# Performance work log

Hardware: AMD Instinct MI355X
Metric: run time of the kernel (lower is better)

The kernel has to match this reference:

```python
import jax, jax.numpy as jnp
import numpy as np

B, S, HID = 1, 2048, 4096
NH, NKV, HD = 32, 8, 128
GROUPS = NH // NKV
ROPE_THETA = 10000.0


def rotate_half(x):
    x1, x2 = jnp.split(x, 2, axis=-1)
    return jnp.concatenate([-x2, x1], axis=-1)


def rope_cos_sin(position_ids, head_dim, dtype):
    # inv_freq: [hd/2]; position_ids: [B, S]
    inv_freq = 1.0 / (ROPE_THETA ** (jnp.arange(0, head_dim, 2, dtype=jnp.float32) / head_dim))
    freqs = position_ids.astype(jnp.float32)[..., None] * inv_freq  # [B, S, hd/2]
    emb = jnp.concatenate([freqs, freqs], axis=-1)                  # [B, S, hd]
    return jnp.cos(emb).astype(dtype), jnp.sin(emb).astype(dtype)


def apply_rope(x, cos, sin):
    # x: [B, H, S, hd]; cos/sin: [B, S, hd] -> broadcast over heads
    return x * cos[:, None] + rotate_half(x) * sin[:, None]


def setup_inputs() -> dict:
    key = jax.random.key(0)
    ks = jax.random.split(key, 5)
    scale = 0.02
    return {
        "hidden_states": jax.random.normal(ks[0], (B, S, HID), dtype=jnp.float32),
        "wq": jax.random.normal(ks[1], (HID, NH * HD), dtype=jnp.float32) * scale,
        "wk": jax.random.normal(ks[2], (HID, NKV * HD), dtype=jnp.float32) * scale,
        "wv": jax.random.normal(ks[3], (HID, NKV * HD), dtype=jnp.float32) * scale,
        "wo": jax.random.normal(ks[4], (NH * HD, HID), dtype=jnp.float32) * scale,
        "position_ids": jnp.arange(S, dtype=jnp.int32)[None, :],
    }


def reference(hidden_states, wq, wk, wv, wo, position_ids):
    bsz, q_len, _ = hidden_states.shape
    # projections (nn.Linear, bias=False)
    q = (hidden_states @ wq).reshape(bsz, q_len, NH, HD).transpose(0, 2, 1, 3)   # [B,NH,S,hd]
    k = (hidden_states @ wk).reshape(bsz, q_len, NKV, HD).transpose(0, 2, 1, 3)  # [B,NKV,S,hd]
    v = (hidden_states @ wv).reshape(bsz, q_len, NKV, HD).transpose(0, 2, 1, 3)
    # RoPE applied to Q and K at global positions (prefill: no past cache)
    cos, sin = rope_cos_sin(position_ids, HD, q.dtype)
    q = apply_rope(q, cos, sin)
    k = apply_rope(k, cos, sin)
    # GQA: expand KV heads to query heads
    k_full = jnp.repeat(k, GROUPS, axis=1)  # [B,NH,S,hd]
    v_full = jnp.repeat(v, GROUPS, axis=1)
    # prefill flash attention == causal SDPA
    logits = jnp.einsum('bhqd,bhkd->bhqk', q, k_full) / jnp.sqrt(jnp.asarray(HD, q.dtype))
    causal = jnp.tril(jnp.ones((q_len, q_len), dtype=bool))
    neg = jnp.asarray(jnp.finfo(q.dtype).min, q.dtype)
    logits = jnp.where(causal[None, None], logits, neg)
    probs = jax.nn.softmax(logits, axis=-1)                     # [B,NH,S,S]
    attn = jnp.einsum('bhqk,bhkd->bhqd', probs, v_full)          # [B,NH,S,hd]
    attn_output = attn.transpose(0, 2, 1, 3).reshape(bsz, q_len, NH * HD) @ wo
    # chunked prefill eviction scores: causal attention probs accumulated over
    # all queries, aggregated per KV head group -> [B, NKV, kv_len]
    accumulated_scores = probs.sum(axis=2).reshape(bsz, NKV, GROUPS, q_len).sum(axis=2)
    return attn_output, accumulated_scores
```

## Files before the change

kernel.cpp:

```cpp
#include <hip/hip_runtime.h>
#include <hip/hip_bf16.h>
#include <cstdint>
#include <cstddef>

#define S_LEN 2048
#define HID_DIM 4096
#define NH 32
#define NKV 8
#define HD 128
#define LOG2E 1.4426950408889634f
#define SCALE 0.08838834764831845f

typedef __attribute__((ext_vector_type(8))) short bf16x8;
typedef __attribute__((ext_vector_type(4))) float f32x4;
typedef __attribute__((ext_vector_type(16))) float f32x16;
typedef __attribute__((ext_vector_type(4))) short short4v;
typedef __attribute__((ext_vector_type(4))) unsigned u32x4;

__device__ __forceinline__ short f2bf(float f) {
  union { float f; unsigned u; } v; v.f = f;
  return (short)((v.u + 0x7fffu + ((v.u >> 16) & 1u)) >> 16);
}
__device__ __forceinline__ float bf2f(short s) {
  union { unsigned u; float f; } v; v.u = ((unsigned)(unsigned short)s) << 16;
  return v.f;
}
__device__ __forceinline__ unsigned cvt_pk_bf16(float lo, float hi) {
  unsigned r;
  asm("v_cvt_pk_bf16_f32 %0, %1, %2" : "=v"(r) : "v"(lo), "v"(hi));
  return r;
}
__device__ __forceinline__ void gld_lds16(const void* g, void* l) {
  __builtin_amdgcn_global_load_lds((const __attribute__((address_space(1))) unsigned*)g,
                                   (__attribute__((address_space(3))) unsigned*)l, 16, 0, 0);
}

#define WAITVM8() asm volatile("s_waitcnt vmcnt(8)" ::: "memory")
#define WAITVM4() asm volatile("s_waitcnt vmcnt(4)" ::: "memory")
#define WAITVM0() asm volatile("s_waitcnt vmcnt(0)" ::: "memory")

__global__ void cvt_kernel(const float* __restrict__ in, short* __restrict__ out, int n) {
  int i = (blockIdx.x * 256 + threadIdx.x) * 4;
  if (i < n) {
    float4 f = *(const float4*)(in + i);
    short4v o = { f2bf(f.x), f2bf(f.y), f2bf(f.z), f2bf(f.w) };
    *(short4v*)(out + i) = o;
  }
}

__global__ void tconv_kernel(const float* __restrict__ in, short* __restrict__ out, int R, int C) {
  __shared__ float tile[32][33];
  int tr = blockIdx.y * 32, tc = blockIdx.x * 32;
  int tx = threadIdx.x & 31, ty = threadIdx.x >> 5;
#pragma unroll
  for (int i = 0; i < 32; i += 8)
    tile[ty + i][tx] = in[(size_t)(tr + ty + i) * C + tc + tx];
  __syncthreads();
#pragma unroll
  for (int i = 0; i < 32; i += 8)
    out[(size_t)(tc + ty + i) * R + tr + tx] = f2bf(tile[tx][ty + i]);
}

template<int MODE>
__global__ __launch_bounds__(256, 4) void gemm_bt_kernel(
    const short* __restrict__ A, const short* __restrict__ Bt,
    void* __restrict__ Cout, int M, int N, int K, int rchunk, int cchunk)
{
  __shared__ short As[2][128 * 32];
  __shared__ short Bs[2][128 * 32];
  const int tid = threadIdx.x;
  const int lane = tid & 63;
  const int w = tid >> 6;
  const int wm = w >> 1, wn = w & 1;
  const int xcd = blockIdx.x & 7;
  const int local = blockIdx.x >> 3;
  const int by = (xcd >> 2) * rchunk + (local % rchunk);
  const int bx = (xcd & 3) * cchunk + (local / rchunk);
  const int m0 = by * 128, n0 = bx * 128;

  auto stage = [&](int bb, int k0) {
#pragma unroll
    for (int rep = 0; rep < 2; rep++) {
      int c = rep * 256 + tid;
      int row = c >> 2, slot = c & 3;
      int gs = slot ^ (row & 3);
      gld_lds16(A + (size_t)(m0 + row) * K + k0 + gs * 8, &As[bb][c * 8]);
      gld_lds16(Bt + (size_t)(n0 + row) * K + k0 + gs * 8, &Bs[bb][c * 8]);
    }
  };

  f32x4 acc[4][4];
#pragma unroll
  for (int i = 0; i < 4; i++)
#pragma unroll
    for (int j = 0; j < 4; j++) acc[i][j] = (f32x4){0.f, 0.f, 0.f, 0.f};

  const int NT = K >> 5;
  stage(0, 0);
  for (int kt = 0; kt < NT; kt++) {
    const int b = kt & 1;
    if (kt + 1 < NT) { stage(b ^ 1, (kt + 1) << 5); WAITVM4(); }
    else             { WAITVM0(); }
    __builtin_amdgcn_s_barrier();

    bf16x8 af[4], bf[4];
#pragma unroll
    for (int ms = 0; ms < 4; ms++) {
      int row = wm * 64 + ms * 16 + (lane & 15);
      af[ms] = *(const bf16x8*)(&As[b][row * 32 + (((lane >> 4) ^ (row & 3)) << 3)]);
    }
#pragma unroll
    for (int ns = 0; ns < 4; ns++) {
      int row = wn * 64 + ns * 16 + (lane & 15);
      bf[ns] = *(const bf16x8*)(&Bs[b][row * 32 + (((lane >> 4) ^ (row & 3)) << 3)]);
    }
#pragma unroll
    for (int ms = 0; ms < 4; ms++)
#pragma unroll
      for (int ns = 0; ns < 4; ns++)
        acc[ms][ns] = __builtin_amdgcn_mfma_f32_16x16x32_bf16(af[ms], bf[ns], acc[ms][ns], 0, 0, 0);

    __builtin_amdgcn_s_barrier();
  }

#pragma unroll
  for (int ms = 0; ms < 4; ms++) {
    int mb = m0 + wm * 64 + ms * 16 + ((lane >> 4) << 2);
#pragma unroll
    for (int ns = 0; ns < 4; ns++) {
      int n = n0 + wn * 64 + ns * 16 + (lane & 15);
      if (MODE == 3) {
        short* o = (short*)Cout;
        if (n < NH * HD) {
          int head = n >> 7, d = n & 127;
#pragma unroll
          for (int r = 0; r < 4; r++)
            o[((size_t)head * M + (mb + r)) * HD + d] = f2bf(acc[ms][ns][r]);
        } else if (n < (NH + NKV) * HD) {
          int head = (n - NH * HD) >> 7, d = n & 127;
          short* ok = o + (size_t)NH * S_LEN * HD;
#pragma unroll
          for (int r = 0; r < 4; r++)
            ok[((size_t)head * M + (mb + r)) * HD + d] = f2bf(acc[ms][ns][r]);
        } else {
          int head = (n - (NH + NKV) * HD) >> 7, d = n & 127;
          short* ov = o + (size_t)(NH + NKV) * S_LEN * HD;
          short4v pk;
#pragma unroll
          for (int r = 0; r < 4; r++) pk[r] = f2bf(acc[ms][ns][r]);
          *(short4v*)(ov + ((size_t)head * HD + d) * M + mb) = pk;
        }
      } else {
        float* o = (float*)Cout;
#pragma unroll
        for (int r = 0; r < 4; r++)
          o[(size_t)(mb + r) * N + n] = acc[ms][ns][r];
      }
    }
  }
}

__global__ void rope_kernel(short* __restrict__ q, short* __restrict__ k,
                            const int* __restrict__ pos_ids) {
  const int s = blockIdx.x;
  const int hh = blockIdx.y * 4 + threadIdx.y;
  const int d = threadIdx.x;
  const float pos = (float)pos_ids[s];
  const float inv = __expf(-(float)d * 0.14391157f);
  float sn, c;
  __sincosf(pos * inv, &sn, &c);
  short* base = (hh < NH) ? (q + ((size_t)hh * S_LEN + s) * HD)
                          : (k + ((size_t)(hh - NH) * S_LEN + s) * HD);
  float x1 = bf2f(base[d]), x2 = bf2f(base[d + 64]);
  base[d] = f2bf(x1 * c - x2 * sn);
  base[d + 64] = f2bf(x2 * c + x1 * sn);
}

__global__ __launch_bounds__(256, 2) void attn_kernel(
    const short* __restrict__ Qr, const short* __restrict__ Kr, const short* __restrict__ Vt,
    short* __restrict__ attn_out, float* __restrict__ scores)
{
  __shared__ short Ks[2][64 * 128];
  __shared__ short Vs[2][128 * 64];
  __shared__ float cs[2048];

  const int tid = threadIdx.x;
  const int lane = tid & 63;
  const int w = tid >> 6;
  const int h2 = lane >> 5;
  const int l31 = lane & 31;
  const int xcd = blockIdx.x & 7;
  const int j = blockIdx.x >> 3;
  const int qt = (j < 32) ? (15 - (j >> 2)) : ((j - 32) >> 2);
  const int h = xcd * 4 + (j & 3);
  const int kvh = xcd;
  const float CS = SCALE * LOG2E;

  const short* KrB = Kr + (size_t)kvh * S_LEN * HD;
  const short* VtB = Vt + (size_t)kvh * HD * S_LEN;

  for (int i = tid; i < 2048; i += 256) cs[i] = 0.f;

  auto stageK = [&](int bb, int t) {
    const int kb2 = t * 64;
#pragma unroll
    for (int rep = 0; rep < 4; rep++) {
      int c = rep * 256 + tid;
      int x = c >> 4, slot = c & 15;
      int key = (x & 0x33) | ((x & 4) << 1) | ((x & 8) >> 1);
      int gs = slot ^ (x & 7);
      gld_lds16(KrB + (size_t)(kb2 + key) * HD + gs * 8, &Ks[bb][c * 8]);
    }
  };
  auto stageV = [&](int bb, int t) {
    const int kb2 = t * 64;
#pragma unroll
    for (int rep = 0; rep < 4; rep++) {
      int c = rep * 256 + tid;
      int d = c >> 3, slot = c & 7;
      int gs = slot ^ (d & 7);
      gld_lds16(VtB + (size_t)d * S_LEN + kb2 + gs * 8, &Vs[bb][c * 8]);
    }
  };

  const int nt = 2 * qt + 2;
  const int qbase = qt * 128 + w * 32;
  const int qglob = qbase + l31;
  const int qmaxw = qbase + 31;

  bf16x8 qf[8];
  {
    const short* qrow = Qr + ((size_t)h * S_LEN + qglob) * HD + h2 * 8;
#pragma unroll
    for (int kc = 0; kc < 8; kc++) qf[kc] = *(const bf16x8*)(qrow + kc * 16);
  }

  f32x16 oacc[4];
#pragma unroll
  for (int i = 0; i < 4; i++) oacc[i] = (f32x16)(0.f);
  float lsum = 0.f;

  stageK(0, 0); stageV(0, 0);
  for (int t = 0; t < nt; t++) {
    const int b = t & 1;
    const int kb = t * 64;
    if (t + 1 < nt) { stageK(b ^ 1, t + 1); stageV(b ^ 1, t + 1); WAITVM8(); }
    else            { WAITVM0(); }
    __builtin_amdgcn_s_barrier();

    if (kb <= qmaxw) {
      f32x16 sf[2];
      sf[0] = (f32x16)(0.f); sf[1] = (f32x16)(0.f);
      __builtin_amdgcn_s_setprio(1);
#pragma unroll
      for (int kc = 0; kc < 8; kc++)
#pragma unroll
        for (int bl = 0; bl < 2; bl++) {
          int x = bl * 32 + l31;
          bf16x8 kf = *(const bf16x8*)(&Ks[b][x * 128 + (((kc * 2 + h2) ^ (lane & 7)) << 3)]);
          sf[bl] = __builtin_amdgcn_mfma_f32_32x32x16_bf16(kf, qf[kc], sf[bl], 0, 0, 0);
        }
      __builtin_amdgcn_s_setprio(0);

      float p[2][16];
      const bool diag = (kb + 63 > qbase);
#pragma unroll
      for (int bl = 0; bl < 2; bl++)
#pragma unroll
        for (int a = 0; a < 4; a++)
#pragma unroll
          for (int cc = 0; cc < 4; cc++) {
            float pv = exp2f(sf[bl][a * 4 + cc] * CS);
            if (diag) {
              int key = kb + bl * 32 + (a >> 1) * 16 + h2 * 8 + (a & 1) * 4 + cc;
              if (key > qglob) pv = 0.f;
            }
            p[bl][a * 4 + cc] = pv;
            lsum += pv;
          }

      bf16x8 pa[4];
#pragma unroll
      for (int s = 0; s < 4; s++) {
        const int bl = s >> 1, base = 8 * (s & 1);
        u32x4 pw;
        pw[0] = cvt_pk_bf16(p[bl][base + 0], p[bl][base + 1]);
        pw[1] = cvt_pk_bf16(p[bl][base + 2], p[bl][base + 3]);
        pw[2] = cvt_pk_bf16(p[bl][base + 4], p[bl][base + 5]);
        pw[3] = cvt_pk_bf16(p[bl][base + 6], p[bl][base + 7]);
        pa[s] = __builtin_bit_cast(bf16x8, pw);
      }

      __builtin_amdgcn_s_setprio(1);
#pragma unroll
      for (int s = 0; s < 4; s++)
#pragma unroll
        for (int db = 0; db < 4; db++) {
          int d = db * 32 + l31;
          bf16x8 vf = *(const bf16x8*)(&Vs[b][d * 64 + (((s * 2 + h2) ^ (lane & 7)) << 3)]);
          oacc[db] = __builtin_amdgcn_mfma_f32_32x32x16_bf16(pa[s], vf, oacc[db], 0, 0, 0);
        }
      __builtin_amdgcn_s_setprio(0);
    }
    __builtin_amdgcn_s_barrier();
  }

  lsum += __shfl_xor(lsum, 32);
  float rlv = 1.f / lsum;
  float rl16[16];
#pragma unroll
  for (int r = 0; r < 16; r++)
    rl16[r] = __shfl(rlv, (r & 3) + 8 * (r >> 2) + 4 * h2);

#pragma unroll
  for (int db = 0; db < 4; db++) {
    int d = db * 32 + l31;
#pragma unroll
    for (int r = 0; r < 16; r++) {
      int qq = qbase + (r & 3) + 8 * (r >> 2) + 4 * h2;
      attn_out[(size_t)qq * HID_DIM + h * HD + d] = f2bf(oacc[db][r] * rl16[r]);
    }
  }

  const int xl = (l31 & 0x13) | ((l31 & 4) << 1) | ((l31 & 8) >> 1);
  stageK(0, 0);
  for (int t = 0; t < nt; t++) {
    const int b = t & 1;
    const int kb = t * 64;
    if (t + 1 < nt) { stageK(b ^ 1, t + 1); WAITVM4(); }
    else            { WAITVM0(); }
    __builtin_amdgcn_s_barrier();

    if (kb <= qmaxw) {
      f32x16 sg[2];
      sg[0] = (f32x16)(0.f); sg[1] = (f32x16)(0.f);
      __builtin_amdgcn_s_setprio(1);
#pragma unroll
      for (int kc = 0; kc < 8; kc++)
#pragma unroll
        for (int bl = 0; bl < 2; bl++) {
          int x = bl * 32 + xl;
          bf16x8 kf = *(const bf16x8*)(&Ks[b][x * 128 + (((kc * 2 + h2) ^ (x & 7)) << 3)]);
          sg[bl] = __builtin_amdgcn_mfma_f32_32x32x16_bf16(qf[kc], kf, sg[bl], 0, 0, 0);
        }
      __builtin_amdgcn_s_setprio(0);

      const bool diag = (kb + 63 > qbase);
#pragma unroll
      for (int bl = 0; bl < 2; bl++) {
        int key = kb + bl * 32 + l31;
        float sum = 0.f;
#pragma unroll
        for (int r = 0; r < 16; r++) {
          float pv = exp2f(sg[bl][r] * CS) * rl16[r];
          if (diag && key > qbase + (r & 3) + 8 * (r >> 2) + 4 * h2) pv = 0.f;
          sum += pv;
        }
        sum += __shfl_xor(sum, 32);
        if (lane < 32) atomicAdd(&cs[key], sum);
      }
    }
    __builtin_amdgcn_s_barrier();
  }

  asm volatile("s_waitcnt lgkmcnt(0)" ::: "memory");
  __builtin_amdgcn_s_barrier();
  const int nk = nt * 64;
  for (int i = tid; i < nk; i += 256)
    atomicAdd(scores + (size_t)kvh * S_LEN + i, cs[i]);
}

extern "C" void kernel_launch(void* const* d_in, const int* in_sizes, int n_in,
                              void* d_out, int out_size, void* d_ws, size_t ws_size,
                              hipStream_t stream) {
  const float* hs = (const float*)d_in[0];
  const float* wq = (const float*)d_in[1];
  const float* wk = (const float*)d_in[2];
  const float* wv = (const float*)d_in[3];
  const float* wo = (const float*)d_in[4];
  const int* pos = (const int*)d_in[5];
  float* out = (float*)d_out;

  char* ws = (char*)d_ws;
  const size_t off_hs   = 0;
  const size_t off_wqT  = off_hs   + (size_t)S_LEN * HID_DIM * 2;
  const size_t off_wkT  = off_wqT  + (size_t)HID_DIM * HID_DIM * 2;
  const size_t off_wvT  = off_wkT  + (size_t)1024 * HID_DIM * 2;
  const size_t off_woT  = off_wvT  + (size_t)1024 * HID_DIM * 2;
  const size_t off_Qr   = off_woT  + (size_t)HID_DIM * HID_DIM * 2;
  const size_t off_Kr   = off_Qr   + (size_t)NH * S_LEN * HD * 2;
  const size_t off_Vt   = off_Kr   + (size_t)NKV * S_LEN * HD * 2;
  const size_t off_attn = off_Vt   + (size_t)NKV * HD * S_LEN * 2;

  short* hsb  = (short*)(ws + off_hs);
  short* wqT  = (short*)(ws + off_wqT);
  short* wkT  = (short*)(ws + off_wkT);
  short* wvT  = (short*)(ws + off_wvT);
  short* woT  = (short*)(ws + off_woT);
  short* Qr   = (short*)(ws + off_Qr);
  short* Kr   = (short*)(ws + off_Kr);
  short* Vt   = (short*)(ws + off_Vt);
  short* attb = (short*)(ws + off_attn);

  cvt_kernel<<<dim3((S_LEN * HID_DIM) / 1024), 256, 0, stream>>>(hs, hsb, S_LEN * HID_DIM);
  tconv_kernel<<<dim3(128, 128), 256, 0, stream>>>(wq, wqT, HID_DIM, HID_DIM);
  tconv_kernel<<<dim3(32, 128), 256, 0, stream>>>(wk, wkT, HID_DIM, 1024);
  tconv_kernel<<<dim3(32, 128), 256, 0, stream>>>(wv, wvT, HID_DIM, 1024);
  tconv_kernel<<<dim3(128, 128), 256, 0, stream>>>(wo, woT, HID_DIM, HID_DIM);

  gemm_bt_kernel<3><<<768, 256, 0, stream>>>(hsb, wqT, Qr, S_LEN, 6144, HID_DIM, 8, 12);

  rope_kernel<<<dim3(S_LEN, 10), dim3(64, 4), 0, stream>>>(Qr, Kr, pos);

  hipMemsetAsync(out + (size_t)S_LEN * HID_DIM, 0, (size_t)NKV * S_LEN * sizeof(float), stream);
  attn_kernel<<<512, 256, 0, stream>>>(Qr, Kr, Vt, attb, out + (size_t)S_LEN * HID_DIM);

  gemm_bt_kernel<2><<<512, 256, 0, stream>>>(attb, woT, out, S_LEN, HID_DIM, HID_DIM, 8, 8);
}
```

Before: 401.7 us.

## Split attention block into paired 64-row q-tiles with key-split waves

Each block now handles two 64-row query tiles (one long and one short, paired so causal work is balanced) instead of one 128-row tile. Each tile's waves are split two ways over query rows and two ways over the keys of every 64-key tile. The partial O and row sums are combined through LDS, which reuses the K/V buffers. The score pass now reads K straight from global memory, with waves striding over key tiles, instead of staging it in LDS. This trades extra LDS reduction, barriers and uncached-pattern global K reads for finer-grained causal balance and smaller per-wave MFMA chains.

```diff
diff --git a/kernel.cpp b/kernel.cpp
--- a/kernel.cpp
+++ b/kernel.cpp
@@ -187,12 +187,14 @@
   const int tid = threadIdx.x;
   const int lane = tid & 63;
   const int w = tid >> 6;
+  const int r = w & 1;
+  const int kh = w >> 1;
   const int h2 = lane >> 5;
   const int l31 = lane & 31;
   const int xcd = blockIdx.x & 7;
   const int j = blockIdx.x >> 3;
-  const int qt = (j < 32) ? (15 - (j >> 2)) : ((j - 32) >> 2);
   const int h = xcd * 4 + (j & 3);
+  const int p = j >> 2;
   const int kvh = xcd;
   const float CS = SCALE * LOG2E;
 
@@ -200,6 +202,10 @@
   const short* VtB = Vt + (size_t)kvh * HD * S_LEN;
 
   for (int i = tid; i < 2048; i += 256) cs[i] = 0.f;
+
+  float* obuf = (float*)Ks;
+  float* lbuf = (float*)Vs;
+  float* rlbuf = lbuf + 64;
 
   auto stageK = [&](int bb, int t) {
     const int kb2 = t * 64;
@@ -223,115 +229,130 @@
     }
   };
 
-  const int nt = 2 * qt + 2;
-  const int qbase = qt * 128 + w * 32;
-  const int qglob = qbase + l31;
-  const int qmaxw = qbase + 31;
-
-  bf16x8 qf[8];
-  {
-    const short* qrow = Qr + ((size_t)h * S_LEN + qglob) * HD + h2 * 8;
-#pragma unroll
-    for (int kc = 0; kc < 8; kc++) qf[kc] = *(const bf16x8*)(qrow + kc * 16);
-  }
-
-  f32x16 oacc[4];
-#pragma unroll
-  for (int i = 0; i < 4; i++) oacc[i] = (f32x16)(0.f);
-  float lsum = 0.f;
-
-  stageK(0, 0); stageV(0, 0);
-  for (int t = 0; t < nt; t++) {
-    const int b = t & 1;
-    const int kb = t * 64;
-    if (t + 1 < nt) { stageK(b ^ 1, t + 1); stageV(b ^ 1, t + 1); WAITVM8(); }
-    else            { WAITVM0(); }
-    __builtin_amdgcn_s_barrier();
-
-    if (kb <= qmaxw) {
-      f32x16 sf[2];
-      sf[0] = (f32x16)(0.f); sf[1] = (f32x16)(0.f);
-      __builtin_amdgcn_s_setprio(1);
-#pragma unroll
-      for (int kc = 0; kc < 8; kc++)
-#pragma unroll
-        for (int bl = 0; bl < 2; bl++) {
-          int x = bl * 32 + l31;
-          bf16x8 kf = *(const bf16x8*)(&Ks[b][x * 128 + (((kc * 2 + h2) ^ (lane & 7)) << 3)]);
-          sf[bl] = __builtin_amdgcn_mfma_f32_32x32x16_bf16(kf, qf[kc], sf[bl], 0, 0, 0);
-        }
-      __builtin_amdgcn_s_setprio(0);
-
-      float p[2][16];
-      const bool diag = (kb + 63 > qbase);
-#pragma unroll
-      for (int bl = 0; bl < 2; bl++)
+  for (int sidx = 0; sidx < 2; sidx++) {
+    const int qt = sidx ? p : (31 - p);
+    const int nt = qt + 1;
+    const int qbase = qt * 64 + r * 32;
+    const int qglob = qbase + l31;
+    const int qmaxw = qbase + 31;
+
+    bf16x8 qf[8];
+    {
+      const short* qrow = Qr + ((size_t)h * S_LEN + qglob) * HD + h2 * 8;
+#pragma unroll
+      for (int kc = 0; kc < 8; kc++) qf[kc] = *(const bf16x8*)(qrow + kc * 16);
+    }
+
+    f32x16 oacc[4];
+#pragma unroll
+    for (int i = 0; i < 4; i++) oacc[i] = (f32x16)(0.f);
+    float lsum = 0.f;
+
+    stageK(0, 0); stageV(0, 0);
+    for (int t = 0; t < nt; t++) {
+      const int b = t & 1;
+      const int kb = t * 64;
+      if (t + 1 < nt) { stageK(b ^ 1, t + 1); stageV(b ^ 1, t + 1); WAITVM8(); }
+      else            { WAITVM0(); }
+      __builtin_amdgcn_s_barrier();
+
+      if (kb <= qmaxw) {
+        f32x16 sf = (f32x16)(0.f);
+        const int x = kh * 32 + l31;
+        __builtin_amdgcn_s_setprio(1);
+#pragma unroll
+        for (int kc = 0; kc < 8; kc++) {
+          bf16x8 kf = *(const bf16x8*)(&Ks[b][x * 128 + (((kc * 2 + h2) ^ (x & 7)) << 3)]);
+          sf = __builtin_amdgcn_mfma_f32_32x32x16_bf16(kf, qf[kc], sf, 0, 0, 0);
+        }
+        __builtin_amdgcn_s_setprio(0);
+
+        float pv16[16];
+        const bool diag = (kb + 63 > qbase);
 #pragma unroll
         for (int a = 0; a < 4; a++)
 #pragma unroll
           for (int cc = 0; cc < 4; cc++) {
-            float pv = exp2f(sf[bl][a * 4 + cc] * CS);
+            float pv = exp2f(sf[a * 4 + cc] * CS);
             if (diag) {
-              int key = kb + bl * 32 + (a >> 1) * 16 + h2 * 8 + (a & 1) * 4 + cc;
+              int key = kb + kh * 32 + (a >> 1) * 16 + h2 * 8 + (a & 1) * 4 + cc;
               if (key > qglob) pv = 0.f;
             }
-            p[bl][a * 4 + cc] = pv;
+            pv16[a * 4 + cc] = pv;
             lsum += pv;
           }
 
-      bf16x8 pa[4];
-#pragma unroll
-      for (int s = 0; s < 4; s++) {
-        const int bl = s >> 1, base = 8 * (s & 1);
-        u32x4 pw;
-        pw[0] = cvt_pk_bf16(p[bl][base + 0], p[bl][base + 1]);
-        pw[1] = cvt_pk_bf16(p[bl][base + 2], p[bl][base + 3]);
-        pw[2] = cvt_pk_bf16(p[bl][base + 4], p[bl][base + 5]);
-        pw[3] = cvt_pk_bf16(p[bl][base + 6], p[bl][base + 7]);
-        pa[s] = __builtin_bit_cast(bf16x8, pw);
+        bf16x8 pa[2];
+#pragma unroll
+        for (int s = 0; s < 2; s++) {
+          u32x4 pw;
+          pw[0] = cvt_pk_bf16(pv16[8 * s + 0], pv16[8 * s + 1]);
+          pw[1] = cvt_pk_bf16(pv16[8 * s + 2], pv16[8 * s + 3]);
+          pw[2] = cvt_pk_bf16(pv16[8 * s + 4], pv16[8 * s + 5]);
+          pw[3] = cvt_pk_bf16(pv16[8 * s + 6], pv16[8 * s + 7]);
+          pa[s] = __builtin_bit_cast(bf16x8, pw);
+        }
+
+        __builtin_amdgcn_s_setprio(1);
+#pragma unroll
+        for (int s = 0; s < 2; s++) {
+          const int g = kh * 2 + s;
+#pragma unroll
+          for (int db = 0; db < 4; db++) {
+            int d = db * 32 + l31;
+            bf16x8 vf = *(const bf16x8*)(&Vs[b][d * 64 + (((g * 2 + h2) ^ (d & 7)) << 3)]);
+            oacc[db] = __builtin_amdgcn_mfma_f32_32x32x16_bf16(pa[s], vf, oacc[db], 0, 0, 0);
+          }
+        }
+        __builtin_amdgcn_s_setprio(0);
       }
-
-      __builtin_amdgcn_s_setprio(1);
-#pragma unroll
-      for (int s = 0; s < 4; s++)
-#pragma unroll
-        for (int db = 0; db < 4; db++) {
-          int d = db * 32 + l31;
-          bf16x8 vf = *(const bf16x8*)(&Vs[b][d * 64 + (((s * 2 + h2) ^ (lane & 7)) << 3)]);
-          oacc[db] = __builtin_amdgcn_mfma_f32_32x32x16_bf16(pa[s], vf, oacc[db], 0, 0, 0);
-        }
-      __builtin_amdgcn_s_setprio(0);
+      __builtin_amdgcn_s_barrier();
+    }
+
+    lsum += __shfl_xor(lsum, 32);
+    if (kh == 0) {
+#pragma unroll
+      for (int db = 0; db < 4; db++)
+#pragma unroll
+        for (int r16 = 0; r16 < 16; r16++) {
+          int crow = (r16 & 3) + 8 * (r16 >> 2) + 4 * h2;
+          obuf[(r * 32 + crow) * 128 + db * 32 + l31] = oacc[db][r16];
+        }
+      if (lane < 32) lbuf[r * 32 + l31] = lsum;
     }
     __builtin_amdgcn_s_barrier();
-  }
-
-  lsum += __shfl_xor(lsum, 32);
-  float rlv = 1.f / lsum;
-  float rl16[16];
-#pragma unroll
-  for (int r = 0; r < 16; r++)
-    rl16[r] = __shfl(rlv, (r & 3) + 8 * (r >> 2) + 4 * h2);
-
-#pragma unroll
-  for (int db = 0; db < 4; db++) {
-    int d = db * 32 + l31;
-#pragma unroll
-    for (int r = 0; r < 16; r++) {
-      int qq = qbase + (r & 3) + 8 * (r >> 2) + 4 * h2;
-      attn_out[(size_t)qq * HID_DIM + h * HD + d] = f2bf(oacc[db][r] * rl16[r]);
-    }
-  }
-
-  const int xl = (l31 & 0x13) | ((l31 & 4) << 1) | ((l31 & 8) >> 1);
-  stageK(0, 0);
-  for (int t = 0; t < nt; t++) {
-    const int b = t & 1;
-    const int kb = t * 64;
-    if (t + 1 < nt) { stageK(b ^ 1, t + 1); WAITVM4(); }
-    else            { WAITVM0(); }
+
+    if (kh == 1) {
+      float ltot = lsum + lbuf[r * 32 + l31];
+      float rlv = 1.f / ltot;
+      float rl16[16];
+#pragma unroll
+      for (int r16 = 0; r16 < 16; r16++)
+        rl16[r16] = __shfl(rlv, (r16 & 3) + 8 * (r16 >> 2) + 4 * h2);
+#pragma unroll
+      for (int db = 0; db < 4; db++) {
+        int d = db * 32 + l31;
+#pragma unroll
+        for (int r16 = 0; r16 < 16; r16++) {
+          int crow = (r16 & 3) + 8 * (r16 >> 2) + 4 * h2;
+          float o = oacc[db][r16] + obuf[(r * 32 + crow) * 128 + d];
+          attn_out[(size_t)(qbase + crow) * HID_DIM + h * HD + d] = f2bf(o * rl16[r16]);
+        }
+      }
+      if (lane < 32) rlbuf[r * 32 + l31] = rlv;
+    }
     __builtin_amdgcn_s_barrier();
 
-    if (kb <= qmaxw) {
+    float rlv = rlbuf[r * 32 + l31];
+    float rl16[16];
+#pragma unroll
+    for (int r16 = 0; r16 < 16; r16++)
+      rl16[r16] = __shfl(rlv, (r16 & 3) + 8 * (r16 >> 2) + 4 * h2);
+    __builtin_amdgcn_s_barrier();
+
+    const int ntw = qmaxw / 64 + 1;
+    for (int t = kh; t < ntw; t += 2) {
+      const int kb = t * 64;
       f32x16 sg[2];
       sg[0] = (f32x16)(0.f); sg[1] = (f32x16)(0.f);
       __builtin_amdgcn_s_setprio(1);
@@ -339,8 +360,7 @@
       for (int kc = 0; kc < 8; kc++)
 #pragma unroll
         for (int bl = 0; bl < 2; bl++) {
-          int x = bl * 32 + xl;
-          bf16x8 kf = *(const bf16x8*)(&Ks[b][x * 128 + (((kc * 2 + h2) ^ (x & 7)) << 3)]);
+          bf16x8 kf = *(const bf16x8*)(KrB + (size_t)(kb + bl * 32 + l31) * HD + kc * 16 + h2 * 8);
           sg[bl] = __builtin_amdgcn_mfma_f32_32x32x16_bf16(qf[kc], kf, sg[bl], 0, 0, 0);
         }
       __builtin_amdgcn_s_setprio(0);
@@ -351,21 +371,20 @@
         int key = kb + bl * 32 + l31;
         float sum = 0.f;
 #pragma unroll
-        for (int r = 0; r < 16; r++) {
-          float pv = exp2f(sg[bl][r] * CS) * rl16[r];
-          if (diag && key > qbase + (r & 3) + 8 * (r >> 2) + 4 * h2) pv = 0.f;
+        for (int r16 = 0; r16 < 16; r16++) {
+          float pv = exp2f(sg[bl][r16] * CS) * rl16[r16];
+          if (diag && key > qbase + (r16 & 3) + 8 * (r16 >> 2) + 4 * h2) pv = 0.f;
           sum += pv;
         }
         sum += __shfl_xor(sum, 32);
         if (lane < 32) atomicAdd(&cs[key], sum);
       }
     }
-    __builtin_amdgcn_s_barrier();
   }
 
   asm volatile("s_waitcnt lgkmcnt(0)" ::: "memory");
   __builtin_amdgcn_s_barrier();
-  const int nk = nt * 64;
+  const int nk = (32 - p) * 64;
   for (int i = tid; i < nk; i += 256)
     atomicAdd(scores + (size_t)kvh * S_LEN + i, cs[i]);
 }
```

After: 391.9 us. 2.4% less time.

## Single-buffer V, raise occupancy, and read K from global in the score pass

Applied to the files above, without the earlier changes.

Drops the V double buffer and the shared column-score array so three blocks can fit per CU instead of two. The main loop is restructured so V for the current tile and K for the next tile load while QK^T and softmax run, with a second barrier before the PV product. The score pass no longer stages K through LDS and no longer synchronises the block: each wave reads K straight from global memory and atomically adds its column sums to the output. The trade-off is more global atomics and uncoalesced global K reads in exchange for fewer barriers and higher occupancy.

```diff
diff --git a/kernel.cpp b/kernel.cpp
--- a/kernel.cpp
+++ b/kernel.cpp
@@ -35,7 +35,6 @@
                                    (__attribute__((address_space(3))) unsigned*)l, 16, 0, 0);
 }
 
-#define WAITVM8() asm volatile("s_waitcnt vmcnt(8)" ::: "memory")
 #define WAITVM4() asm volatile("s_waitcnt vmcnt(4)" ::: "memory")
 #define WAITVM0() asm volatile("s_waitcnt vmcnt(0)" ::: "memory")
 
@@ -176,13 +175,12 @@
   base[d + 64] = f2bf(x2 * c + x1 * sn);
 }
 
-__global__ __launch_bounds__(256, 2) void attn_kernel(
+__global__ __launch_bounds__(256, 3) void attn_kernel(
     const short* __restrict__ Qr, const short* __restrict__ Kr, const short* __restrict__ Vt,
     short* __restrict__ attn_out, float* __restrict__ scores)
 {
   __shared__ short Ks[2][64 * 128];
-  __shared__ short Vs[2][128 * 64];
-  __shared__ float cs[2048];
+  __shared__ short Vs[128 * 64];
 
   const int tid = threadIdx.x;
   const int lane = tid & 63;
@@ -191,15 +189,18 @@
   const int l31 = lane & 31;
   const int xcd = blockIdx.x & 7;
   const int j = blockIdx.x >> 3;
-  const int qt = (j < 32) ? (15 - (j >> 2)) : ((j - 32) >> 2);
   const int h = xcd * 4 + (j & 3);
+  const int qt = 15 - (j >> 2);
   const int kvh = xcd;
   const float CS = SCALE * LOG2E;
 
   const short* KrB = Kr + (size_t)kvh * S_LEN * HD;
   const short* VtB = Vt + (size_t)kvh * HD * S_LEN;
 
-  for (int i = tid; i < 2048; i += 256) cs[i] = 0.f;
+  const int nt = 2 * qt + 2;
+  const int qbase = qt * 128 + w * 32;
+  const int qglob = qbase + l31;
+  const int qmaxw = qbase + 31;
 
   auto stageK = [&](int bb, int t) {
     const int kb2 = t * 64;
@@ -212,21 +213,16 @@
       gld_lds16(KrB + (size_t)(kb2 + key) * HD + gs * 8, &Ks[bb][c * 8]);
     }
   };
-  auto stageV = [&](int bb, int t) {
+  auto stageV = [&](int t) {
     const int kb2 = t * 64;
 #pragma unroll
     for (int rep = 0; rep < 4; rep++) {
       int c = rep * 256 + tid;
       int d = c >> 3, slot = c & 7;
       int gs = slot ^ (d & 7);
-      gld_lds16(VtB + (size_t)d * S_LEN + kb2 + gs * 8, &Vs[bb][c * 8]);
+      gld_lds16(VtB + (size_t)d * S_LEN + kb2 + gs * 8, &Vs[c * 8]);
     }
   };
-
-  const int nt = 2 * qt + 2;
-  const int qbase = qt * 128 + w * 32;
-  const int qglob = qbase + l31;
-  const int qmaxw = qbase + 31;
 
   bf16x8 qf[8];
   {
@@ -240,15 +236,19 @@
   for (int i = 0; i < 4; i++) oacc[i] = (f32x16)(0.f);
   float lsum = 0.f;
 
-  stageK(0, 0); stageV(0, 0);
+  stageK(0, 0);
   for (int t = 0; t < nt; t++) {
     const int b = t & 1;
     const int kb = t * 64;
-    if (t + 1 < nt) { stageK(b ^ 1, t + 1); stageV(b ^ 1, t + 1); WAITVM8(); }
-    else            { WAITVM0(); }
+    WAITVM0();
     __builtin_amdgcn_s_barrier();
 
-    if (kb <= qmaxw) {
+    stageV(t);
+    if (t + 1 < nt) stageK(b ^ 1, t + 1);
+
+    bf16x8 pa[4];
+    const bool live = (kb <= qmaxw);
+    if (live) {
       f32x16 sf[2];
       sf[0] = (f32x16)(0.f); sf[1] = (f32x16)(0.f);
       __builtin_amdgcn_s_setprio(1);
@@ -257,7 +257,7 @@
 #pragma unroll
         for (int bl = 0; bl < 2; bl++) {
           int x = bl * 32 + l31;
-          bf16x8 kf = *(const bf16x8*)(&Ks[b][x * 128 + (((kc * 2 + h2) ^ (lane & 7)) << 3)]);
+          bf16x8 kf = *(const bf16x8*)(&Ks[b][x * 128 + (((kc * 2 + h2) ^ (x & 7)) << 3)]);
           sf[bl] = __builtin_amdgcn_mfma_f32_32x32x16_bf16(kf, qf[kc], sf[bl], 0, 0, 0);
         }
       __builtin_amdgcn_s_setprio(0);
@@ -279,7 +279,6 @@
             lsum += pv;
           }
 
-      bf16x8 pa[4];
 #pragma unroll
       for (int s = 0; s < 4; s++) {
         const int bl = s >> 1, base = 8 * (s & 1);
@@ -290,84 +289,74 @@
         pw[3] = cvt_pk_bf16(p[bl][base + 6], p[bl][base + 7]);
         pa[s] = __builtin_bit_cast(bf16x8, pw);
       }
-
+    }
+
+    if (t + 1 < nt) WAITVM4();
+    else           WAITVM0();
+    __builtin_amdgcn_s_barrier();
+
+    if (live) {
       __builtin_amdgcn_s_setprio(1);
 #pragma unroll
       for (int s = 0; s < 4; s++)
 #pragma unroll
         for (int db = 0; db < 4; db++) {
           int d = db * 32 + l31;
-          bf16x8 vf = *(const bf16x8*)(&Vs[b][d * 64 + (((s * 2 + h2) ^ (lane & 7)) << 3)]);
+          bf16x8 vf = *(const bf16x8*)(&Vs[d * 64 + (((s * 2 + h2) ^ (d & 7)) << 3)]);
           oacc[db] = __builtin_amdgcn_mfma_f32_32x32x16_bf16(pa[s], vf, oacc[db], 0, 0, 0);
         }
       __builtin_amdgcn_s_setprio(0);
     }
-    __builtin_amdgcn_s_barrier();
   }
 
   lsum += __shfl_xor(lsum, 32);
   float rlv = 1.f / lsum;
   float rl16[16];
 #pragma unroll
-  for (int r = 0; r < 16; r++)
-    rl16[r] = __shfl(rlv, (r & 3) + 8 * (r >> 2) + 4 * h2);
+  for (int r16 = 0; r16 < 16; r16++)
+    rl16[r16] = __shfl(rlv, (r16 & 3) + 8 * (r16 >> 2) + 4 * h2);
 
 #pragma unroll
   for (int db = 0; db < 4; db++) {
     int d = db * 32 + l31;
 #pragma unroll
-    for (int r = 0; r < 16; r++) {
-      int qq = qbase + (r & 3) + 8 * (r >> 2) + 4 * h2;
-      attn_out[(size_t)qq * HID_DIM + h * HD + d] = f2bf(oacc[db][r] * rl16[r]);
-    }
-  }
-
-  const int xl = (l31 & 0x13) | ((l31 & 4) << 1) | ((l31 & 8) >> 1);
-  stageK(0, 0);
-  for (int t = 0; t < nt; t++) {
-    const int b = t & 1;
+    for (int r16 = 0; r16 < 16; r16++) {
+      int qq = qbase + (r16 & 3) + 8 * (r16 >> 2) + 4 * h2;
+      attn_out[(size_t)qq * HID_DIM + h * HD + d] = f2bf(oacc[db][r16] * rl16[r16]);
+    }
+  }
+
+  float* sc = scores + (size_t)kvh * S_LEN;
+  const int ntw = qmaxw / 64 + 1;
+  for (int t = 0; t < ntw; t++) {
     const int kb = t * 64;
-    if (t + 1 < nt) { stageK(b ^ 1, t + 1); WAITVM4(); }
-    else            { WAITVM0(); }
-    __builtin_amdgcn_s_barrier();
-
-    if (kb <= qmaxw) {
-      f32x16 sg[2];
-      sg[0] = (f32x16)(0.f); sg[1] = (f32x16)(0.f);
-      __builtin_amdgcn_s_setprio(1);
-#pragma unroll
-      for (int kc = 0; kc < 8; kc++)
-#pragma unroll
-        for (int bl = 0; bl < 2; bl++) {
-          int x = bl * 32 + xl;
-          bf16x8 kf = *(const bf16x8*)(&Ks[b][x * 128 + (((kc * 2 + h2) ^ (x & 7)) << 3)]);
-          sg[bl] = __builtin_amdgcn_mfma_f32_32x32x16_bf16(qf[kc], kf, sg[bl], 0, 0, 0);
-        }
-      __builtin_amdgcn_s_setprio(0);
-
-      const bool diag = (kb + 63 > qbase);
+    f32x16 sg[2];
+    sg[0] = (f32x16)(0.f); sg[1] = (f32x16)(0.f);
+    __builtin_amdgcn_s_setprio(1);
+#pragma unroll
+    for (int kc = 0; kc < 8; kc++)
 #pragma unroll
       for (int bl = 0; bl < 2; bl++) {
-        int key = kb + bl * 32 + l31;
-        float sum = 0.f;
-#pragma unroll
-        for (int r = 0; r < 16; r++) {
-          float pv = exp2f(sg[bl][r] * CS) * rl16[r];
-          if (diag && key > qbase + (r & 3) + 8 * (r >> 2) + 4 * h2) pv = 0.f;
-          sum += pv;
-        }
-        sum += __shfl_xor(sum, 32);
-        if (lane < 32) atomicAdd(&cs[key], sum);
+        bf16x8 kf = *(const bf16x8*)(KrB + (size_t)(kb + bl * 32 + l31) * HD + kc * 16 + h2 * 8);
+        sg[bl] = __builtin_amdgcn_mfma_f32_32x32x16_bf16(qf[kc], kf, sg[bl], 0, 0, 0);
       }
-    }
-    __builtin_amdgcn_s_barrier();
-  }
-
-  asm volatile("s_waitcnt lgkmcnt(0)" ::: "memory");
-  __builtin_amdgcn_s_barrier();
-  const int nk = nt * 64;
-  for (int i = tid; i < nk; i += 256)
-    atomicAdd(scores + (size_t)kvh * S_LEN + i, cs[i]);
+    __builtin_amdgcn_s_setprio(0);
+
+    const bool diag = (kb + 63 > qbase);
+#pragma unroll
+    for (int bl = 0; bl < 2; bl++) {
+      int key = kb + bl * 32 + l31;
+      float sum = 0.f;
+#pragma unroll
+      for (int r16 = 0; r16 < 16; r16++) {
+        float pv = exp2f(sg[bl][r16] * CS) * rl16[r16];
+        if (diag && key > qbase + (r16 & 3) + 8 * (r16 >> 2) + 4 * h2) pv = 0.f;
+        sum += pv;
+      }
+      sum += __shfl_xor(sum, 32);
+      if (lane < 32) atomicAdd(&sc[key], sum);
+    }
+  }
 }
 
 extern "C" void kernel_launch(void* const* d_in, const int* in_sizes, int n_in,
```

New measurement: 463.0 us. +15.3%, slower.
